# Kernel optimization log

Measured on AMD Instinct MI355X. Metric: run time of the kernel, lower is better.

The kernel has to match this reference:

```python
import jax, jax.numpy as jnp
import numpy as np

C = 3  # RGB channels

# Scharr kernels, depthwise: shape [C_out, C_in/groups, kh, kw] = [C, 1, 3, 3]
_KX = np.array([[-3., 0., 3.], [-10., 0., 10.], [-3., 0., 3.]], dtype=np.float32)
_KY = np.array([[-3., -10., -3.], [0., 0., 0.], [3., 10., 3.]], dtype=np.float32)
KERNEL_X = jnp.tile(jnp.asarray(_KX)[None, None], (C, 1, 1, 1))
KERNEL_Y = jnp.tile(jnp.asarray(_KY)[None, None], (C, 1, 1, 1))


def _depthwise3x3(img, kernel):
    # img: [B, C, H, W]; kernel: [C, 1, 3, 3]; groups=C, stride 1, padding 1
    return jax.lax.conv_general_dilated(
        img, kernel,
        window_strides=(1, 1),
        padding=((1, 1), (1, 1)),
        dimension_numbers=('NCHW', 'OIHW', 'NCHW'),
        feature_group_count=C)


def _scharr_grad(img):
    gx = _depthwise3x3(img, KERNEL_X)
    gy = _depthwise3x3(img, KERNEL_Y)
    return jnp.abs(gx) + jnp.abs(gy)


def setup_inputs() -> dict:
    key = jax.random.key(0)
    kx, kg = jax.random.split(key)
    x = jax.random.uniform(kx, (16, 3, 512, 512), dtype=jnp.float32)
    gt = jax.random.uniform(kg, (16, 3, 512, 512), dtype=jnp.float32)
    return {"x": x, "gt": gt}


def reference(x, gt):
    loss = jnp.abs(_scharr_grad(x) - _scharr_grad(gt))
    return jnp.mean(loss)  # size_average=True
```

## Files before the change

kernel.cpp:

```cpp
#include <hip/hip_runtime.h>

#define Wd 512
#define Hd 512
#define NIMG 48
#define RB 16
#define LR (RB + 2)
#define NBLK (NIMG * (Hd / RB))
constexpr float INV_N = 1.0f / (float)((long long)NIMG * Hd * Wd);

__device__ __forceinline__ void gload_lds16(const float* g, float* l) {
    __builtin_amdgcn_global_load_lds(
        (const __attribute__((address_space(1))) void*)g,
        (__attribute__((address_space(3))) void*)l, 16, 0, 0);
}

__device__ __forceinline__ float scharr_pix(const float r0[10], const float r1[10],
                                            const float r2[10], int j) {
    float tl = r0[j], tm = r0[j + 1], tr = r0[j + 2];
    float ml = r1[j],                  mr = r1[j + 2];
    float bl = r2[j], bm = r2[j + 1], br = r2[j + 2];
    float gx = 3.f * (tr - tl) + 10.f * (mr - ml) + 3.f * (br - bl);
    float gy = 3.f * (bl - tl) + 10.f * (bm - tm) + 3.f * (br - tr);
    return fabsf(gx) + fabsf(gy);
}

__device__ __forceinline__ void lds_row(const float* __restrict__ row, int lane,
                                        float r[10]) {
    float4 b0 = *reinterpret_cast<const float4*>(row + lane * 8);
    float4 b1 = *reinterpret_cast<const float4*>(row + lane * 8 + 4);
    r[1] = b0.x; r[2] = b0.y; r[3] = b0.z; r[4] = b0.w;
    r[5] = b1.x; r[6] = b1.y; r[7] = b1.z; r[8] = b1.w;
    float lv = __shfl_up(b1.w, 1, 64);
    float rv = __shfl_down(b0.x, 1, 64);
    r[0] = (lane > 0)  ? lv : 0.f;
    r[9] = (lane < 63) ? rv : 0.f;
}

__global__ void __launch_bounds__(256)
scharr_loss_kernel(const float* __restrict__ x, const float* __restrict__ gt,
                   float* __restrict__ partials) {
    __shared__ float lb[2][LR][Wd];
    __shared__ float ws[4];

    int wid  = threadIdx.x >> 6;
    int lane = threadIdx.x & 63;

    int b   = blockIdx.x;
    int swz = (b & 7) * (NBLK / 8) + (b >> 3);
    int img = swz >> 5;
    int h0  = (swz & 31) * RB;

    const float* __restrict__ xb = x  + (size_t)img * Hd * Wd;
    const float* __restrict__ gb = gt + (size_t)img * Hd * Wd;

    int is   = wid >> 1;
    int half = wid & 1;
    const float* __restrict__ sb = is ? gb : xb;
    #pragma unroll
    for (int t = 0; t < LR; ++t) {
        int gh = h0 - 1 + t;
        float* dst = &lb[is][t][half * 256];
        if ((unsigned)gh < (unsigned)Hd) {
            gload_lds16(sb + (size_t)gh * Wd + half * 256 + lane * 4, dst);
        } else {
            *reinterpret_cast<float4*>(dst + lane * 4) =
                make_float4(0.f, 0.f, 0.f, 0.f);
        }
    }
    __syncthreads();

    int r0 = wid * 4;
    float rx[3][10], rg[3][10];
    lds_row(&lb[0][r0][0],     lane, rx[0]);
    lds_row(&lb[0][r0 + 1][0], lane, rx[1]);
    lds_row(&lb[1][r0][0],     lane, rg[0]);
    lds_row(&lb[1][r0 + 1][0], lane, rg[1]);

    float sum = 0.f;
    #pragma unroll
    for (int i = 0; i < 4; ++i) {
        const int c0 = i % 3, c1 = (i + 1) % 3, c2 = (i + 2) % 3;
        lds_row(&lb[0][r0 + i + 2][0], lane, rx[c2]);
        lds_row(&lb[1][r0 + i + 2][0], lane, rg[c2]);
        #pragma unroll
        for (int j = 0; j < 8; ++j) {
            float a = scharr_pix(rx[c0], rx[c1], rx[c2], j);
            float g = scharr_pix(rg[c0], rg[c1], rg[c2], j);
            sum += fabsf(a - g);
        }
    }

    #pragma unroll
    for (int off = 32; off > 0; off >>= 1)
        sum += __shfl_down(sum, off, 64);
    if (lane == 0) ws[wid] = sum;
    __syncthreads();
    if (threadIdx.x == 0)
        partials[blockIdx.x] = ws[0] + ws[1] + ws[2] + ws[3];
}

__global__ void __launch_bounds__(256)
reduce_partials_kernel(const float* __restrict__ partials, float* __restrict__ out) {
    float s = 0.f;
    #pragma unroll
    for (int k = 0; k < NBLK / 256; ++k)
        s += partials[k * 256 + threadIdx.x];
    #pragma unroll
    for (int off = 32; off > 0; off >>= 1)
        s += __shfl_down(s, off, 64);
    __shared__ float ws[4];
    int lane = threadIdx.x & 63;
    int wid  = threadIdx.x >> 6;
    if (lane == 0) ws[wid] = s;
    __syncthreads();
    if (threadIdx.x == 0)
        out[0] = (ws[0] + ws[1] + ws[2] + ws[3]) * INV_N;
}

extern "C" void kernel_launch(void* const* d_in, const int* in_sizes, int n_in,
                              void* d_out, int out_size, void* d_ws, size_t ws_size,
                              hipStream_t stream) {
    const float* x  = (const float*)d_in[0];
    const float* gt = (const float*)d_in[1];
    float* out      = (float*)d_out;
    float* partials = (float*)d_ws;

    scharr_loss_kernel<<<NBLK, 256, 0, stream>>>(x, gt, partials);
    reduce_partials_kernel<<<1, 256, 0, stream>>>(partials, out);
}
```

Baseline: 24.98 us.

## Use persistent blocks with double-buffered LDS tiles and atomic final reduction

```diff
diff --git a/kernel.cpp b/kernel.cpp
--- a/kernel.cpp
+++ b/kernel.cpp
@@ -5,7 +5,9 @@
 #define NIMG 48
 #define RB 16
 #define LR (RB + 2)
-#define NBLK (NIMG * (Hd / RB))
+#define NT (NIMG * (Hd / RB))
+#define NBLK 256
+#define TPB (NT / NBLK)
 constexpr float INV_N = 1.0f / (float)((long long)NIMG * Hd * Wd);
 
 __device__ __forceinline__ void gload_lds16(const float* g, float* l) {
@@ -38,56 +40,64 @@
 
 __global__ void __launch_bounds__(256)
 scharr_loss_kernel(const float* __restrict__ x, const float* __restrict__ gt,
-                   float* __restrict__ partials) {
-    __shared__ float lb[2][LR][Wd];
+                   float* __restrict__ out) {
+    __shared__ float lb[2][2][LR][Wd];
     __shared__ float ws[4];
 
     int wid  = threadIdx.x >> 6;
     int lane = threadIdx.x & 63;
-
-    int b   = blockIdx.x;
-    int swz = (b & 7) * (NBLK / 8) + (b >> 3);
-    int img = swz >> 5;
-    int h0  = (swz & 31) * RB;
-
-    const float* __restrict__ xb = x  + (size_t)img * Hd * Wd;
-    const float* __restrict__ gb = gt + (size_t)img * Hd * Wd;
-
     int is   = wid >> 1;
     int half = wid & 1;
-    const float* __restrict__ sb = is ? gb : xb;
-    #pragma unroll
-    for (int t = 0; t < LR; ++t) {
-        int gh = h0 - 1 + t;
-        float* dst = &lb[is][t][half * 256];
-        if ((unsigned)gh < (unsigned)Hd) {
-            gload_lds16(sb + (size_t)gh * Wd + half * 256 + lane * 4, dst);
-        } else {
-            *reinterpret_cast<float4*>(dst + lane * 4) =
-                make_float4(0.f, 0.f, 0.f, 0.f);
+    const float* __restrict__ sb = (is ? gt : x);
+
+    int t0 = blockIdx.x * TPB;
+
+    auto stage = [&](int ti, int buf) {
+        int img = ti >> 5;
+        int h0  = (ti & 31) * RB;
+        const float* __restrict__ ib = sb + (size_t)img * Hd * Wd;
+        #pragma unroll
+        for (int t = 0; t < LR; ++t) {
+            int gh = h0 - 1 + t;
+            float* dst = &lb[buf][is][t][half * 256];
+            if ((unsigned)gh < (unsigned)Hd) {
+                gload_lds16(ib + (size_t)gh * Wd + half * 256 + lane * 4, dst);
+            } else {
+                *reinterpret_cast<float4*>(dst + lane * 4) =
+                    make_float4(0.f, 0.f, 0.f, 0.f);
+            }
         }
-    }
+    };
+
+    float sum = 0.f;
+    stage(t0, 0);
     __syncthreads();
 
-    int r0 = wid * 4;
-    float rx[3][10], rg[3][10];
-    lds_row(&lb[0][r0][0],     lane, rx[0]);
-    lds_row(&lb[0][r0 + 1][0], lane, rx[1]);
-    lds_row(&lb[1][r0][0],     lane, rg[0]);
-    lds_row(&lb[1][r0 + 1][0], lane, rg[1]);
+    #pragma unroll
+    for (int k = 0; k < TPB; ++k) {
+        if (k + 1 < TPB) stage(t0 + k + 1, (k + 1) & 1);
 
-    float sum = 0.f;
-    #pragma unroll
-    for (int i = 0; i < 4; ++i) {
-        const int c0 = i % 3, c1 = (i + 1) % 3, c2 = (i + 2) % 3;
-        lds_row(&lb[0][r0 + i + 2][0], lane, rx[c2]);
-        lds_row(&lb[1][r0 + i + 2][0], lane, rg[c2]);
+        const int bf = k & 1;
+        int r0 = wid * 4;
+        float rx[3][10], rg[3][10];
+        lds_row(&lb[bf][0][r0][0],     lane, rx[0]);
+        lds_row(&lb[bf][0][r0 + 1][0], lane, rx[1]);
+        lds_row(&lb[bf][1][r0][0],     lane, rg[0]);
+        lds_row(&lb[bf][1][r0 + 1][0], lane, rg[1]);
         #pragma unroll
-        for (int j = 0; j < 8; ++j) {
-            float a = scharr_pix(rx[c0], rx[c1], rx[c2], j);
-            float g = scharr_pix(rg[c0], rg[c1], rg[c2], j);
-            sum += fabsf(a - g);
+        for (int i = 0; i < 4; ++i) {
+            const int c0 = i % 3, c1 = (i + 1) % 3, c2 = (i + 2) % 3;
+            lds_row(&lb[bf][0][r0 + i + 2][0], lane, rx[c2]);
+            lds_row(&lb[bf][1][r0 + i + 2][0], lane, rg[c2]);
+            #pragma unroll
+            for (int j = 0; j < 8; ++j) {
+                float a = scharr_pix(rx[c0], rx[c1], rx[c2], j);
+                float g = scharr_pix(rg[c0], rg[c1], rg[c2], j);
+                sum += fabsf(a - g);
+            }
         }
+
+        __syncthreads();
     }
 
     #pragma unroll
@@ -96,25 +106,7 @@
     if (lane == 0) ws[wid] = sum;
     __syncthreads();
     if (threadIdx.x == 0)
-        partials[blockIdx.x] = ws[0] + ws[1] + ws[2] + ws[3];
-}
-
-__global__ void __launch_bounds__(256)
-reduce_partials_kernel(const float* __restrict__ partials, float* __restrict__ out) {
-    float s = 0.f;
-    #pragma unroll
-    for (int k = 0; k < NBLK / 256; ++k)
-        s += partials[k * 256 + threadIdx.x];
-    #pragma unroll
-    for (int off = 32; off > 0; off >>= 1)
-        s += __shfl_down(s, off, 64);
-    __shared__ float ws[4];
-    int lane = threadIdx.x & 63;
-    int wid  = threadIdx.x >> 6;
-    if (lane == 0) ws[wid] = s;
-    __syncthreads();
-    if (threadIdx.x == 0)
-        out[0] = (ws[0] + ws[1] + ws[2] + ws[3]) * INV_N;
+        atomicAdd(out, (ws[0] + ws[1] + ws[2] + ws[3]) * INV_N);
 }
 
 extern "C" void kernel_launch(void* const* d_in, const int* in_sizes, int n_in,
@@ -123,8 +115,8 @@
     const float* x  = (const float*)d_in[0];
     const float* gt = (const float*)d_in[1];
     float* out      = (float*)d_out;
-    float* partials = (float*)d_ws;
 
-    scharr_loss_kernel<<<NBLK, 256, 0, stream>>>(x, gt, partials);
-    reduce_partials_kernel<<<1, 256, 0, stream>>>(partials, out);
+    hipMemsetAsync(out, 0, sizeof(float), stream);
+
+    scharr_loss_kernel<<<NBLK, 256, 0, stream>>>(x, gt, out);
 }
```

Result: slower. 70.88 us (+183.8%).

## Use 512-thread blocks and fold partial reduction into atomicAdd

Applied to the files above, without the earlier changes.

```diff
diff --git a/kernel.cpp b/kernel.cpp
--- a/kernel.cpp
+++ b/kernel.cpp
@@ -36,11 +36,11 @@
     r[9] = (lane < 63) ? rv : 0.f;
 }
 
-__global__ void __launch_bounds__(256)
+__global__ void __launch_bounds__(512)
 scharr_loss_kernel(const float* __restrict__ x, const float* __restrict__ gt,
-                   float* __restrict__ partials) {
+                   float* __restrict__ out) {
     __shared__ float lb[2][LR][Wd];
-    __shared__ float ws[4];
+    __shared__ float ws[8];
 
     int wid  = threadIdx.x >> 6;
     int lane = threadIdx.x & 63;
@@ -53,13 +53,16 @@
     const float* __restrict__ xb = x  + (size_t)img * Hd * Wd;
     const float* __restrict__ gb = gt + (size_t)img * Hd * Wd;
 
-    int is   = wid >> 1;
-    int half = wid & 1;
-    const float* __restrict__ sb = is ? gb : xb;
     #pragma unroll
-    for (int t = 0; t < LR; ++t) {
-        int gh = h0 - 1 + t;
-        float* dst = &lb[is][t][half * 256];
+    for (int t = 0; t < 9; ++t) {
+        int c    = wid + t * 8;
+        int im   = (c >= 36) ? 1 : 0;
+        int cc   = c - im * 36;
+        int row  = cc >> 1;
+        int half = cc & 1;
+        int gh   = h0 - 1 + row;
+        const float* __restrict__ sb = im ? gb : xb;
+        float* dst = &lb[im][row][half * 256];
         if ((unsigned)gh < (unsigned)Hd) {
             gload_lds16(sb + (size_t)gh * Wd + half * 256 + lane * 4, dst);
         } else {
@@ -69,19 +72,19 @@
     }
     __syncthreads();
 
-    int r0 = wid * 4;
+    int lr = wid * 2;
     float rx[3][10], rg[3][10];
-    lds_row(&lb[0][r0][0],     lane, rx[0]);
-    lds_row(&lb[0][r0 + 1][0], lane, rx[1]);
-    lds_row(&lb[1][r0][0],     lane, rg[0]);
-    lds_row(&lb[1][r0 + 1][0], lane, rg[1]);
+    lds_row(&lb[0][lr][0],     lane, rx[0]);
+    lds_row(&lb[0][lr + 1][0], lane, rx[1]);
+    lds_row(&lb[1][lr][0],     lane, rg[0]);
+    lds_row(&lb[1][lr + 1][0], lane, rg[1]);
 
     float sum = 0.f;
     #pragma unroll
-    for (int i = 0; i < 4; ++i) {
+    for (int i = 0; i < 2; ++i) {
         const int c0 = i % 3, c1 = (i + 1) % 3, c2 = (i + 2) % 3;
-        lds_row(&lb[0][r0 + i + 2][0], lane, rx[c2]);
-        lds_row(&lb[1][r0 + i + 2][0], lane, rg[c2]);
+        lds_row(&lb[0][lr + i + 2][0], lane, rx[c2]);
+        lds_row(&lb[1][lr + i + 2][0], lane, rg[c2]);
         #pragma unroll
         for (int j = 0; j < 8; ++j) {
             float a = scharr_pix(rx[c0], rx[c1], rx[c2], j);
@@ -95,26 +98,11 @@
         sum += __shfl_down(sum, off, 64);
     if (lane == 0) ws[wid] = sum;
     __syncthreads();
-    if (threadIdx.x == 0)
-        partials[blockIdx.x] = ws[0] + ws[1] + ws[2] + ws[3];
-}
-
-__global__ void __launch_bounds__(256)
-reduce_partials_kernel(const float* __restrict__ partials, float* __restrict__ out) {
-    float s = 0.f;
-    #pragma unroll
-    for (int k = 0; k < NBLK / 256; ++k)
-        s += partials[k * 256 + threadIdx.x];
-    #pragma unroll
-    for (int off = 32; off > 0; off >>= 1)
-        s += __shfl_down(s, off, 64);
-    __shared__ float ws[4];
-    int lane = threadIdx.x & 63;
-    int wid  = threadIdx.x >> 6;
-    if (lane == 0) ws[wid] = s;
-    __syncthreads();
-    if (threadIdx.x == 0)
-        out[0] = (ws[0] + ws[1] + ws[2] + ws[3]) * INV_N;
+    if (threadIdx.x == 0) {
+        float s = ws[0] + ws[1] + ws[2] + ws[3]
+                + ws[4] + ws[5] + ws[6] + ws[7];
+        atomicAdd(out, s * INV_N);
+    }
 }
 
 extern "C" void kernel_launch(void* const* d_in, const int* in_sizes, int n_in,
@@ -123,8 +111,8 @@
     const float* x  = (const float*)d_in[0];
     const float* gt = (const float*)d_in[1];
     float* out      = (float*)d_out;
-    float* partials = (float*)d_ws;
 
-    scharr_loss_kernel<<<NBLK, 256, 0, stream>>>(x, gt, partials);
-    reduce_partials_kernel<<<1, 256, 0, stream>>>(partials, out);
+    hipMemsetAsync(out, 0, sizeof(float), stream);
+
+    scharr_loss_kernel<<<NBLK, 512, 0, stream>>>(x, gt, out);
 }
```

Result: slower. 37.19 us (+48.9%).
